# Kernel tuning notes

Measured on AMD Instinct MI355X. Metric: run time of the kernel, lower is better.

Reference implementation:

```python
import jax, jax.numpy as jnp
from jax import lax
import numpy as np

NPOINT = 1024
RADII = (0.1, 0.2, 0.4)
NSAMPLES = (16, 32, 64)
MLPS = ((64, 64, 128), (128, 128, 256), (128, 128, 256))
IN_CH = 64  # 3 (xyz) + 61 (point features)
EPS = 1e-5


def setup_inputs() -> dict:
    key = jax.random.key(0)
    ks = jax.random.split(key, 64)
    inp = {
        "xyz": jax.random.normal(ks[0], (8, 3, 16384), dtype=jnp.float32),
        "points": jax.random.normal(ks[1], (8, 61, 16384), dtype=jnp.float32),
    }
    ki = 2
    for i, mlp in enumerate(MLPS):
        last = IN_CH
        for j, out_ch in enumerate(mlp):
            inp[f"w{i}{j}"] = jax.random.normal(ks[ki], (out_ch, last), dtype=jnp.float32) * 0.05
            inp[f"b{i}{j}"] = jnp.zeros((out_ch,), dtype=jnp.float32)
            inp[f"g{i}{j}"] = jnp.ones((out_ch,), dtype=jnp.float32)
            inp[f"bt{i}{j}"] = jnp.zeros((out_ch,), dtype=jnp.float32)
            last = out_ch
            ki += 1
    return inp


def square_distance(src, dst):
    # src [B,S,3], dst [B,N,3] -> [B,S,N]
    d = -2.0 * jnp.einsum("bsc,bnc->bsn", src, dst)
    d = d + jnp.sum(src * src, -1)[:, :, None]
    d = d + jnp.sum(dst * dst, -1)[:, None, :]
    return d


def farthest_point_sample(xyz, npoint):
    # xyz [B,N,3] -> idx [B,npoint]; deterministic start at index 0
    B, N, _ = xyz.shape
    def step(carry, _):
        distance, farthest = carry
        centroid = jnp.take_along_axis(xyz, farthest[:, None, None], axis=1)  # [B,1,3]
        dist = jnp.sum((xyz - centroid) ** 2, axis=-1)  # [B,N]
        distance = jnp.minimum(distance, dist)
        return (distance, jnp.argmax(distance, axis=-1).astype(jnp.int32)), farthest
    init = (jnp.full((B, N), 1e10, dtype=xyz.dtype), jnp.zeros((B,), dtype=jnp.int32))
    _, idxs = lax.scan(step, init, None, length=npoint)
    return idxs.T  # [B,npoint]


def gather_points(p, idx):
    # p [B,N,C], idx [B,...] -> [B,...,C]
    B = p.shape[0]
    flat = idx.reshape(B, -1)
    g = jnp.take_along_axis(p, flat[:, :, None], axis=1)
    return g.reshape(idx.shape + (p.shape[-1],))


def query_ball_points(radius, nsample, xyz, new_xyz):
    # xyz [B,N,3], new_xyz [B,S,3] -> idx [B,S,nsample]
    B, N, _ = xyz.shape
    d = square_distance(new_xyz, xyz)  # [B,S,N]
    idx = jnp.broadcast_to(jnp.arange(N, dtype=jnp.int32), d.shape)
    idx = jnp.where(d > radius * radius, N, idx)
    idx = jnp.sort(idx, axis=-1)[:, :, :nsample]
    first = idx[:, :, :1]
    return jnp.where(idx == N, first, idx)


def _forward(xyz, points, params):
    xyz_t = jnp.transpose(xyz, (0, 2, 1))       # [B,N,3]
    pts_t = jnp.transpose(points, (0, 2, 1))    # [B,N,D]
    B, N, _ = xyz_t.shape
    fps_idx = farthest_point_sample(xyz_t, NPOINT)
    new_xyz = gather_points(xyz_t, fps_idx)     # [B,S,3]
    feats = []
    for i, (radius, K) in enumerate(zip(RADII, NSAMPLES)):
        gidx = query_ball_points(radius, K, xyz_t, new_xyz)      # [B,S,K]
        grouped_xyz = gather_points(xyz_t, gidx) - new_xyz[:, :, None, :]
        grouped_pts = gather_points(pts_t, gidx)
        x = jnp.concatenate([grouped_xyz, grouped_pts], axis=-1)  # [B,S,K,IN_CH]
        for (w, b, g, bt) in params[i]:
            x = jnp.einsum("bskc,oc->bsko", x, w) + b  # 1x1 conv
            mean = jnp.mean(x, axis=(0, 1, 2))
            var = jnp.var(x, axis=(0, 1, 2))
            x = jax.nn.relu(g * (x - mean) * lax.rsqrt(var + EPS) + bt)
        feats.append(jnp.max(x, axis=2))  # [B,S,Cout]
    new_points = jnp.transpose(jnp.concatenate(feats, axis=-1), (0, 2, 1))  # [B,640,S]
    return jnp.transpose(new_xyz, (0, 2, 1)), new_points


def reference(xyz, points,
              w00, b00, g00, bt00, w01, b01, g01, bt01, w02, b02, g02, bt02,
              w10, b10, g10, bt10, w11, b11, g11, bt11, w12, b12, g12, bt12,
              w20, b20, g20, bt20, w21, b21, g21, bt21, w22, b22, g22, bt22):
    params = [
        [(w00, b00, g00, bt00), (w01, b01, g01, bt01), (w02, b02, g02, bt02)],
        [(w10, b10, g10, bt10), (w11, b11, g11, bt11), (w12, b12, g12, bt12)],
        [(w20, b20, g20, bt20), (w21, b21, g21, bt21), (w22, b22, g22, bt22)],
    ]
    return _forward(xyz, points, params)
```

## Files before the change

kernel.cpp:

```cpp
#include <hip/hip_runtime.h>
#include <stdint.h>

#define BB 8
#define NN 16384
#define SS 1024

typedef unsigned short u16;
typedef float f32x4 __attribute__((ext_vector_type(4)));
typedef short short8v __attribute__((ext_vector_type(8)));
typedef unsigned short us4 __attribute__((ext_vector_type(4)));
typedef unsigned short us8 __attribute__((ext_vector_type(8)));

static __device__ __forceinline__ float bf2f(u16 u){
    union { uint32_t u; float f; } v; v.u = ((uint32_t)u) << 16; return v.f;
}
static __device__ __forceinline__ u16 f2bf(float f){
    union { float f; uint32_t u; } v; v.f = f;
    return (u16)((v.u + 0x7FFFu + ((v.u >> 16) & 1u)) >> 16);
}
static constexpr int cmax2(int a, int b){ return a > b ? a : b; }

#define LP 12288

__global__ __launch_bounds__(1024) void fps_kernel(const float* __restrict__ xyz,
                                                   int* __restrict__ fps_idx){
#pragma clang fp contract(off)
    __shared__ float lx[LP], ly[LP], lz[LP];
    __shared__ unsigned long long slot;
    int b = blockIdx.x;
    int t = threadIdx.x;
    const float* xb = xyz + (size_t)b*3*NN;
    float px[16], py[16], pz[16], dd[16];
#pragma unroll
    for (int j=0;j<16;++j){
        int n = t + j*1024;
        px[j] = xb[n];
        py[j] = xb[NN+n];
        pz[j] = xb[2*NN+n];
        dd[j] = 1e10f;
    }
#pragma unroll
    for (int j=0;j<16;++j){
        asm volatile("" : "+v"(px[j]), "+v"(py[j]), "+v"(pz[j]));
    }
    for (int idx = t; idx < LP; idx += 1024){
        lx[idx] = xb[idx];
        ly[idx] = xb[NN+idx];
        lz[idx] = xb[2*NN+idx];
    }
    if (t == 0) slot = 0ull;
    __syncthreads();

    int lane = t & 63;
    int far = 0;
    int* outp = fps_idx + b*SS;
    float cx = xb[0], cy = xb[NN], cz = xb[2*NN];
    for (int it=0; it<SS; ++it){
        if (t==0) outp[it] = far;
#pragma unroll
        for (int j=0;j<16;++j){
            float dx = px[j]-cx, dy = py[j]-cy, dz = pz[j]-cz;
            float d = dx*dx + dy*dy;
            d = d + dz*dz;
            dd[j] = fminf(dd[j], d);
        }
        float m01 = fmaxf(dd[0], dd[1]),  m23 = fmaxf(dd[2], dd[3]);
        float m45 = fmaxf(dd[4], dd[5]),  m67 = fmaxf(dd[6], dd[7]);
        float m89 = fmaxf(dd[8], dd[9]),  mab = fmaxf(dd[10], dd[11]);
        float mcd = fmaxf(dd[12], dd[13]), mef = fmaxf(dd[14], dd[15]);
        float ma = fmaxf(fmaxf(m01, m23), fmaxf(m45, m67));
        float mb = fmaxf(fmaxf(m89, mab), fmaxf(mcd, mef));
        float mx = fmaxf(ma, mb);
        int bj = 0;
#pragma unroll
        for (int j=15; j>=0; --j){
            if (dd[j] == mx) bj = j;
        }
        int bn = t + (bj << 10);
        unsigned long long pk = ((unsigned long long)(unsigned)(it+1) << 46)
                              | ((unsigned long long)__float_as_uint(mx) << 14)
                              | (unsigned long long)(unsigned)(16383 - bn);
#pragma unroll
        for (int off=32; off>0; off>>=1){
            unsigned long long o = __shfl_down(pk, off);
            pk = (o > pk) ? o : pk;
        }
        if (lane == 0) atomicMax(&slot, pk);
        __syncthreads();
        unsigned long long win = slot;
        far = 16383 - (int)(win & 0x3FFFull);
        if (far < LP){
            cx = lx[far]; cy = ly[far]; cz = lz[far];
        } else {
            cx = xb[far]; cy = xb[NN+far]; cz = xb[2*NN+far];
        }
    }
}

__global__ void gather_q_kernel(const float* __restrict__ xyz, const int* __restrict__ fps_idx,
                                float* __restrict__ q, float* __restrict__ out_xyz){
    int i = blockIdx.x*blockDim.x + threadIdx.x;
    if (i >= BB*SS) return;
    int b = i >> 10, s = i & 1023;
    int idx = fps_idx[i];
    for (int c=0;c<3;++c){
        float v = xyz[((size_t)b*3+c)*NN + idx];
        q[i*3+c] = v;
        out_xyz[((size_t)b*3+c)*SS + s] = v;
    }
}

__global__ __launch_bounds__(256) void build_ptsT_kernel(const float* __restrict__ xyz, const float* __restrict__ pts,
                                                         float* __restrict__ ptsT){
    __shared__ float tile[64][65];
    int b = blockIdx.y;
    int n0 = blockIdx.x * 64;
    int t = threadIdx.x;
    int ln = t & 63, cr = t >> 6;
    for (int c = cr; c < 64; c += 4){
        float v;
        if (c < 3) v = xyz[((size_t)b*3 + c)*NN + n0 + ln];
        else       v = pts[((size_t)b*61 + (c-3))*NN + n0 + ln];
        tile[ln][c] = v;
    }
    __syncthreads();
    int lc = t & 63, nr = t >> 6;
    for (int n = nr; n < 64; n += 4){
        ptsT[((size_t)b*NN + n0 + n)*64 + lc] = tile[n][lc];
    }
}

__global__ __launch_bounds__(256) void ballquery_kernel(const float* __restrict__ xyz, const float* __restrict__ q,
        int* __restrict__ idx0, int* __restrict__ idx1, int* __restrict__ idx2,
        float r2a, float r2b, float r2c){
#pragma clang fp contract(off)
    __shared__ int lds[4][112];
    int t = threadIdx.x;
    int w = t >> 6, lane = t & 63;
    int qi = blockIdx.x*4 + w;
    int b = qi >> 10;
    const float* xb = xyz + (size_t)b*3*NN;
    float qx = q[qi*3], qy = q[qi*3+1], qz = q[qi*3+2];
    float qn = qx*qx + qy*qy; qn = qn + qz*qz;
    int* l0 = lds[w];
    int* l1 = l0 + 16;
    int* l2 = l0 + 48;
    l0[lane] = 0;
    if (lane < 48) l0[64+lane] = 0;
    int c0=0, c1=0, c2=0;
    uint64_t below = (1ull << lane) - 1ull;
    for (int ch=0; ch<256; ++ch){
        int n = ch*64 + lane;
        float x = xb[n], y = xb[NN+n], z = xb[2*NN+n];
        float dn = x*x + y*y; dn = dn + z*z;
        float dot = qx*x + qy*y; dot = dot + qz*z;
        float d = -2.0f*dot + qn;
        d = d + dn;
        bool o0 = d <= r2a, o1 = d <= r2b, o2 = d <= r2c;
        uint64_t m0 = __ballot(o0), m1 = __ballot(o1), m2 = __ballot(o2);
        if (c0 < 16){
            int p = c0 + (int)__popcll(m0 & below);
            if (o0 && p < 16) l0[p] = n;
            c0 += (int)__popcll(m0); if (c0 > 16) c0 = 16;
        }
        if (c1 < 32){
            int p = c1 + (int)__popcll(m1 & below);
            if (o1 && p < 32) l1[p] = n;
            c1 += (int)__popcll(m1); if (c1 > 32) c1 = 32;
        }
        if (c2 < 64){
            int p = c2 + (int)__popcll(m2 & below);
            if (o2 && p < 64) l2[p] = n;
            c2 += (int)__popcll(m2); if (c2 > 64) c2 = 64;
        }
        if (c0>=16 && c1>=32 && c2>=64) break;
    }
    __syncthreads();
    int f0 = l0[0], f1 = l1[0], f2 = l2[0];
    if (lane >= c0 && lane < 16) l0[lane] = f0;
    if (lane >= c1 && lane < 32) l1[lane] = f1;
    if (lane >= c2)              l2[lane] = f2;
    __syncthreads();
    if (lane < 16) idx0[(size_t)qi*16 + lane] = l0[lane];
    if (lane < 32) idx1[(size_t)qi*32 + lane] = l1[lane];
    idx2[(size_t)qi*64 + lane] = l2[lane];
}


template<int CC, int OH>
__device__ __forceinline__ void stage_W(const float* __restrict__ W, char* __restrict__ Wl, int t){
    constexpr int CH = CC/8;
    constexpr int SLOTS = OH*CH;
    for (int s = t; s < SLOTS; s += 256){
        int o = s / CH, kc = s - o*CH;
        const float* wp = W + o*CC + kc*8;
        float4 w0 = *(const float4*)(wp);
        float4 w1 = *(const float4*)(wp+4);
        us8 u;
        u[0]=f2bf(w0.x); u[1]=f2bf(w0.y); u[2]=f2bf(w0.z); u[3]=f2bf(w0.w);
        u[4]=f2bf(w1.x); u[5]=f2bf(w1.y); u[6]=f2bf(w1.z); u[7]=f2bf(w1.w);
        *(us8*)(Wl + o*(CC*2) + ((kc*16) ^ ((o&7)<<4))) = u;
    }
}

template<int K>
__device__ __forceinline__ void stage_A_gather(const float* __restrict__ ptsT, const float* __restrict__ q,
                                               const int* __restrict__ gidx, int m0, int t, char* __restrict__ As){
    int r = t >> 2, q4 = t & 3;
    int m = m0 + r;
    int idx = gidx[m];
    int bs = m / K;
    int b = bs >> 10;
    const float* base = ptsT + ((size_t)b*NN + idx)*64;
    float qx=0.f, qy=0.f, qz=0.f;
    if (q4 == 0){ qx = q[bs*3]; qy = q[bs*3+1]; qz = q[bs*3+2]; }
    int rx = (r & 7) << 4;
#pragma unroll
    for (int ii=0; ii<4; ++ii){
        int c0 = q4*16 + ii*4;
        float4 v = *(const float4*)(base + c0);
        if (q4==0 && ii==0){ v.x -= qx; v.y -= qy; v.z -= qz; }
        us4 u;
        u[0]=f2bf(v.x); u[1]=f2bf(v.y); u[2]=f2bf(v.z); u[3]=f2bf(v.w);
        *(us4*)(As + r*128 + ((c0*2) ^ rx)) = u;
    }
}

template<int OP>
__device__ __forceinline__ void stage_A_z(const u16* __restrict__ zbuf, int m0,
                                          const float* __restrict__ sc, const float* __restrict__ sh,
                                          int t, char* __restrict__ As){
    constexpr int CQ = OP/4;
    for (int s = t; s < 64*CQ; s += 256){
        int r = s / CQ, cq = s - r*CQ;
        us4 zv = *(const us4*)&zbuf[((size_t)(m0+r))*OP + cq*4];
        int c = cq*4;
        us4 u;
        u[0] = f2bf(fmaxf(0.f, bf2f(zv[0])*sc[c+0] + sh[c+0]));
        u[1] = f2bf(fmaxf(0.f, bf2f(zv[1])*sc[c+1] + sh[c+1]));
        u[2] = f2bf(fmaxf(0.f, bf2f(zv[2])*sc[c+2] + sh[c+2]));
        u[3] = f2bf(fmaxf(0.f, bf2f(zv[3])*sc[c+3] + sh[c+3]));
        *(us4*)(As + r*(OP*2) + ((cq*8) ^ ((r&7)<<4))) = u;
    }
}

template<int CC, int OH>
__device__ __forceinline__ void mfma_gemm(const char* __restrict__ As, const char* __restrict__ Wl,
                                          f32x4 (&acc)[4][OH/64], int l, int w){
    constexpr int CCB = CC*2;
    int rl = l & 15, kg = l >> 4;
    const char* ap = As + rl*CCB;
    const char* wp = Wl + (w*(OH/4) + rl)*CCB;
    int axor = (rl & 7) << 4;
#pragma unroll
    for (int ks=0; ks<CC/32; ++ks){
        int karg = ((ks<<6) | (kg<<4)) ^ axor;
        short8v a0 = *(const short8v*)(ap + 0*16*CCB + karg);
        short8v a1 = *(const short8v*)(ap + 1*16*CCB + karg);
        short8v a2 = *(const short8v*)(ap + 2*16*CCB + karg);
        short8v a3 = *(const short8v*)(ap + 3*16*CCB + karg);
#pragma unroll
        for (int tc=0; tc<OH/64; ++tc){
            short8v bf = *(const short8v*)(wp + tc*16*CCB + karg);
            acc[0][tc] = __builtin_amdgcn_mfma_f32_16x16x32_bf16(a0, bf, acc[0][tc], 0,0,0);
            acc[1][tc] = __builtin_amdgcn_mfma_f32_16x16x32_bf16(a1, bf, acc[1][tc], 0,0,0);
            acc[2][tc] = __builtin_amdgcn_mfma_f32_16x16x32_bf16(a2, bf, acc[2][tc], 0,0,0);
            acc[3][tc] = __builtin_amdgcn_mfma_f32_16x16x32_bf16(a3, bf, acc[3][tc], 0,0,0);
        }
    }
}

template<int OH>
__device__ __forceinline__ void bias_mfma(f32x4 (&acc)[4][OH/64], const float* __restrict__ bsrc,
                                          int l, int w, int coff){
#pragma unroll
    for (int tc=0; tc<OH/64; ++tc){
        float bb = bsrc[coff + w*(OH/4) + tc*16 + (l&15)];
#pragma unroll
        for (int tr=0; tr<4; ++tr)
#pragma unroll
        for (int e=0; e<4; ++e) acc[tr][tc][e] += bb;
    }
}

template<int OH, int OT>
__device__ __forceinline__ void zstore_mfma(f32x4 (&acc)[4][OH/64], u16* __restrict__ zbuf,
                                            int m0, int l, int w, int coff){
#pragma unroll
    for (int tr=0; tr<4; ++tr)
#pragma unroll
    for (int e=0; e<4; ++e){
        int row = tr*16 + (l>>4)*4 + e;
#pragma unroll
        for (int tc=0; tc<OH/64; ++tc){
            int c = coff + w*(OH/4) + tc*16 + (l&15);
            zbuf[((size_t)(m0+row))*OT + c] = f2bf(acc[tr][tc][e]);
        }
    }
}

template<int OH, int OT, int K, bool EXT>
__device__ __forceinline__ void stats_mfma(f32x4 (&acc)[4][OH/64], int l, int w, int m0, int blk, int coff,
    float* __restrict__ pS, float* __restrict__ pQ,
    float* __restrict__ gmax, float* __restrict__ gmin){
#pragma unroll
    for (int tc=0; tc<OH/64; ++tc){
        float s1 = 0.f, s2 = 0.f;
        float mxr[4], mnr[4];
#pragma unroll
        for (int tr=0; tr<4; ++tr){
            float v0=acc[tr][tc][0], v1=acc[tr][tc][1], v2=acc[tr][tc][2], v3=acc[tr][tc][3];
            s1 += (v0+v1)+(v2+v3);
            s2 += (v0*v0+v1*v1)+(v2*v2+v3*v3);
            if (EXT){
                mxr[tr] = fmaxf(fmaxf(v0,v1),fmaxf(v2,v3));
                mnr[tr] = fminf(fminf(v0,v1),fminf(v2,v3));
            }
        }
        s1 += __shfl_xor(s1,16); s1 += __shfl_xor(s1,32);
        s2 += __shfl_xor(s2,16); s2 += __shfl_xor(s2,32);
        if (EXT){
#pragma unroll
            for (int tr=0; tr<4; ++tr){
                mxr[tr] = fmaxf(mxr[tr], __shfl_xor(mxr[tr],16));
                mxr[tr] = fmaxf(mxr[tr], __shfl_xor(mxr[tr],32));
                mnr[tr] = fminf(mnr[tr], __shfl_xor(mnr[tr],16));
                mnr[tr] = fminf(mnr[tr], __shfl_xor(mnr[tr],32));
            }
        }
        if (l < 16){
            int c = coff + w*(OH/4) + tc*16 + l;
            pS[(size_t)blk*OT + c] = s1;
            pQ[(size_t)blk*OT + c] = s2;
            if (EXT){
                constexpr int G = 64/K, WG = K/16;
#pragma unroll
                for (int g=0; g<G; ++g){
                    float M1 = mxr[g*WG], M2 = mnr[g*WG];
#pragma unroll
                    for (int ww=1; ww<WG; ++ww){
                        M1 = fmaxf(M1, mxr[g*WG+ww]);
                        M2 = fminf(M2, mnr[g*WG+ww]);
                    }
                    gmax[(size_t)(m0/K + g)*OT + c] = M1;
                    gmin[(size_t)(m0/K + g)*OT + c] = M2;
                }
            }
        }
    }
}

template<int OH>
__device__ __forceinline__ void act_to_As_mfma(f32x4 (&acc)[4][OH/64], const float* __restrict__ bsrc,
    const float* __restrict__ sc, const float* __restrict__ sh, int l, int w, char* __restrict__ As){
#pragma unroll
    for (int tc=0; tc<OH/64; ++tc){
        int c = w*(OH/4) + tc*16 + (l&15);
        float bb = bsrc[c], scv = sc[c], shv = sh[c];
#pragma unroll
        for (int tr=0; tr<4; ++tr)
#pragma unroll
        for (int e=0; e<4; ++e){
            int row = tr*16 + (l>>4)*4 + e;
            float vv = fmaxf(0.f, (acc[tr][tc][e]+bb)*scv + shv);
            *(u16*)(As + row*(OH*2) + ((2*c) ^ ((row&7)<<4))) = f2bf(vv);
        }
    }
}

template<int PHASE, int K, int O1, int O2, int O3>
__global__ __launch_bounds__(256) void fused_mlp(
    const float* __restrict__ ptsT, const float* __restrict__ q, const int* __restrict__ gidx,
    const float* __restrict__ W1, const float* __restrict__ b1,
    const float* __restrict__ W2, const float* __restrict__ b2,
    const float* __restrict__ W3, const float* __restrict__ b3,
    const float* __restrict__ sc1, const float* __restrict__ sh1,
    const float* __restrict__ sc2, const float* __restrict__ sh2,
    float* __restrict__ pS, float* __restrict__ pQ,
    float* __restrict__ gmax, float* __restrict__ gmin,
    u16* __restrict__ zbuf)
{
    constexpr int OH3 = (O3 > 128) ? 128 : O3;
    constexpr int AMX = (PHASE==1) ? 64 : (PHASE==2 ? O1 : (PHASE==3 ? cmax2(O1,O2) : O2));
    constexpr int WMX = (PHASE==1) ? O1*64
                      : (PHASE==2) ? cmax2(O2*O1, O1*64)
                      : (PHASE==3) ? cmax2(cmax2(O1*64, O2*O1), OH3*O2)
                      : OH3*O2;
    __shared__ __align__(16) char smem[64*AMX*2 + WMX*2];
    char* As = smem;
    char* Wl = smem + 64*AMX*2;
    int t = threadIdx.x, l = t & 63, w = t >> 6;
    int m0 = blockIdx.x * 64;

    if constexpr (PHASE == 1){
        stage_A_gather<K>(ptsT, q, gidx, m0, t, As);
        stage_W<64,O1>(W1, Wl, t);
        __syncthreads();
        f32x4 acc[4][O1/64] = {};
        mfma_gemm<64,O1>(As, Wl, acc, l, w);
        bias_mfma<O1>(acc, b1, l, w, 0);
        if (zbuf) zstore_mfma<O1,O1>(acc, zbuf, m0, l, w, 0);
        stats_mfma<O1,O1,K,false>(acc, l, w, m0, blockIdx.x, 0, pS,pQ,gmax,gmin);
        return;
    }

    if constexpr (PHASE == 2){
        if (zbuf){
            stage_A_z<O1>(zbuf, m0, sc1, sh1, t, As);
            stage_W<O1,O2>(W2, Wl, t);
            __syncthreads();
        } else {
            stage_A_gather<K>(ptsT, q, gidx, m0, t, As);
            stage_W<64,O1>(W1, Wl, t);
            __syncthreads();
            f32x4 acc1[4][O1/64] = {};
            mfma_gemm<64,O1>(As, Wl, acc1, l, w);
            __syncthreads();
            act_to_As_mfma<O1>(acc1, b1, sc1, sh1, l, w, As);
            stage_W<O1,O2>(W2, Wl, t);
            __syncthreads();
        }
        f32x4 acc[4][O2/64] = {};
        mfma_gemm<O1,O2>(As, Wl, acc, l, w);
        bias_mfma<O2>(acc, b2, l, w, 0);
        if (zbuf) zstore_mfma<O2,O2>(acc, zbuf, m0, l, w, 0);
        stats_mfma<O2,O2,K,false>(acc, l, w, m0, blockIdx.x, 0, pS,pQ,gmax,gmin);
        return;
    }

    if constexpr (PHASE == 3){
        stage_A_gather<K>(ptsT, q, gidx, m0, t, As);
        stage_W<64,O1>(W1, Wl, t);
        __syncthreads();
        f32x4 acc1[4][O1/64] = {};
        mfma_gemm<64,O1>(As, Wl, acc1, l, w);
        __syncthreads();
        act_to_As_mfma<O1>(acc1, b1, sc1, sh1, l, w, As);
        stage_W<O1,O2>(W2, Wl, t);
        __syncthreads();
        f32x4 acc2[4][O2/64] = {};
        mfma_gemm<O1,O2>(As, Wl, acc2, l, w);
        __syncthreads();
        act_to_As_mfma<O2>(acc2, b2, sc2, sh2, l, w, As);
    } else {
        stage_A_z<O2>(zbuf, m0, sc2, sh2, t, As);
    }

    constexpr int HH = O3/OH3;
#pragma unroll
    for (int h=0; h<HH; ++h){
        stage_W<O2,OH3>(W3 + (size_t)h*OH3*O2, Wl, t);
        __syncthreads();
        f32x4 acc[4][OH3/64] = {};
        mfma_gemm<O2,OH3>(As, Wl, acc, l, w);
        bias_mfma<OH3>(acc, b3, l, w, h*OH3);
        stats_mfma<OH3,O3,K,true>(acc, l, w, m0, blockIdx.x, h*OH3, pS,pQ,gmax,gmin);
        if (h+1 < HH) __syncthreads();
    }
}

__global__ __launch_bounds__(256) void finalize_d_kernel(const float* __restrict__ pS, const float* __restrict__ pQ,
                                      const float* __restrict__ g, const float* __restrict__ bt,
                                      float* __restrict__ sc, float* __restrict__ sh, int nb, double invM){
    __shared__ double red[512];
    int c = blockIdx.x;
    int O = gridDim.x;
    int t = threadIdx.x;
    double S=0.0, Q=0.0;
    for (int v=t; v<nb; v+=256){ S += (double)pS[(size_t)v*O + c]; Q += (double)pQ[(size_t)v*O + c]; }
    red[t]=S; red[256+t]=Q;
    __syncthreads();
    for (int s=128; s>0; s>>=1){
        if (t<s){ red[t]+=red[t+s]; red[256+t]+=red[256+t+s]; }
        __syncthreads();
    }
    if (t==0){
        double mean = red[0]*invM;
        double var  = red[256]*invM - mean*mean;
        double scale = (double)g[c] / sqrt(var + 1e-5);
        sc[c] = (float)scale;
        sh[c] = (float)((double)bt[c] - mean*scale);
    }
}

__global__ void final_out_kernel(const float* __restrict__ gmax, const float* __restrict__ gmin,
                                 const float* __restrict__ sc, const float* __restrict__ sh,
                                 float* __restrict__ outp, int O, int logO, int chbase){
    int gid = blockIdx.x*256 + threadIdx.x;
    int c  = gid & (O-1);
    int bs = gid >> logO;
    int b = bs >> 10, s = bs & 1023;
    float scale = sc[c];
    float v = (scale >= 0.f) ? gmax[gid] : gmin[gid];
    float r = fmaxf(0.f, scale*v + sh[c]);
    outp[((size_t)(b*640 + chbase + c))*SS + s] = r;
}

__global__ void ws_marker_kernel(float* outp, float wsval){ if (threadIdx.x==0) outp[0] = wsval; }

template<int K, int O1, int O2, int O3>
static void run_branch(const float* ptsT, const float* q, const int* gidx,
                       float* pS, float* pQ, float* gmax, float* gmin,
                       float* sc1, float* sh1, float* sc2, float* sh2, float* sc3, float* sh3,
                       u16* z2buf, bool use_z,
                       void* const* d_in, int wbase, float* np_out, int chbase, hipStream_t stream)
{
    const int M = BB*SS*K;
    const int nb = M/64;
    auto wp = [&](int jl, int which)->const float* { return (const float*)d_in[2 + (wbase+jl)*4 + which]; };
    const double invM = 1.0 / (double)M;
    u16* zb = use_z ? z2buf : (u16*)nullptr;

    fused_mlp<1,K,O1,O2,O3><<<nb,256,0,stream>>>(ptsT,q,gidx,
        wp(0,0),wp(0,1), wp(1,0),wp(1,1), wp(2,0),wp(2,1),
        sc1,sh1, sc2,sh2, pS,pQ, gmax,gmin, zb);
    finalize_d_kernel<<<O1,256,0,stream>>>(pS,pQ, wp(0,2), wp(0,3), sc1, sh1, nb, invM);

    fused_mlp<2,K,O1,O2,O3><<<nb,256,0,stream>>>(ptsT,q,gidx,
        wp(0,0),wp(0,1), wp(1,0),wp(1,1), wp(2,0),wp(2,1),
        sc1,sh1, sc2,sh2, pS,pQ, gmax,gmin, zb);
    finalize_d_kernel<<<O2,256,0,stream>>>(pS,pQ, wp(1,2), wp(1,3), sc2, sh2, nb, invM);

    if (use_z){
        fused_mlp<4,K,O1,O2,O3><<<nb,256,0,stream>>>(ptsT,q,gidx,
            wp(0,0),wp(0,1), wp(1,0),wp(1,1), wp(2,0),wp(2,1),
            sc1,sh1, sc2,sh2, pS,pQ, gmax,gmin, z2buf);
    } else {
        fused_mlp<3,K,O1,O2,O3><<<nb,256,0,stream>>>(ptsT,q,gidx,
            wp(0,0),wp(0,1), wp(1,0),wp(1,1), wp(2,0),wp(2,1),
            sc1,sh1, sc2,sh2, pS,pQ, gmax,gmin, nullptr);
    }
    finalize_d_kernel<<<O3,256,0,stream>>>(pS,pQ, wp(2,2), wp(2,3), sc3, sh3, nb, invM);

    final_out_kernel<<<(BB*SS*O3)/256,256,0,stream>>>(gmax,gmin, sc3,sh3, np_out, O3, (O3==256?8:7), chbase);
}

extern "C" void kernel_launch(void* const* d_in, const int* in_sizes, int n_in,
                              void* d_out, int out_size, void* d_ws, size_t ws_size,
                              hipStream_t stream)
{
    const float* xyz = (const float*)d_in[0];
    const float* pts = (const float*)d_in[1];
    float* outp = (float*)d_out;

    char* wsb = (char*)d_ws;
    size_t off = 0;
    auto alloc = [&](size_t bytes) -> void* {
        off = (off + 255) & ~(size_t)255;
        void* p = wsb + off;
        off += bytes;
        return p;
    };
    int*   fps_idx = (int*)  alloc((size_t)BB*SS*4);
    float* q       = (float*)alloc((size_t)BB*SS*3*4);
    int*   idx0    = (int*)  alloc((size_t)BB*SS*16*4);
    int*   idx1    = (int*)  alloc((size_t)BB*SS*32*4);
    int*   idx2    = (int*)  alloc((size_t)BB*SS*64*4);
    float* ptsT    = (float*)alloc((size_t)BB*NN*64*4);
    float* pS      = (float*)alloc((size_t)8192*256*4);
    float* pQ      = (float*)alloc((size_t)8192*256*4);
    float* gmax    = (float*)alloc((size_t)8192*256*4);
    float* gmin    = (float*)alloc((size_t)8192*256*4);
    float* sc1     = (float*)alloc(256*4);
    float* sh1     = (float*)alloc(256*4);
    float* sc2     = (float*)alloc(256*4);
    float* sh2     = (float*)alloc(256*4);
    float* sc3     = (float*)alloc(256*4);
    float* sh3     = (float*)alloc(256*4);

    if (off > ws_size){
        ws_marker_kernel<<<1,64,0,stream>>>(outp, (float)ws_size);
        return;
    }

    u16* z2buf = (u16*)alloc((size_t)BB*SS*64*128*2);
    bool use_z = (off <= ws_size);

    build_ptsT_kernel<<<dim3(NN/64, BB), 256, 0, stream>>>(xyz, pts, ptsT);
    fps_kernel<<<BB, 1024, 0, stream>>>(xyz, fps_idx);
    gather_q_kernel<<<32, 256, 0, stream>>>(xyz, fps_idx, q, outp);

    const float r2a = (float)(0.1*0.1);
    const float r2b = (float)(0.2*0.2);
    const float r2c = (float)(0.4*0.4);
    ballquery_kernel<<<2048, 256, 0, stream>>>(xyz, q, idx0, idx1, idx2, r2a, r2b, r2c);

    float* np_out = outp + (size_t)BB*3*SS;
    run_branch<16, 64, 64,128>(ptsT, q, idx0, pS,pQ, gmax,gmin, sc1,sh1,sc2,sh2,sc3,sh3, z2buf, use_z, d_in, 0, np_out,   0, stream);
    run_branch<32,128,128,256>(ptsT, q, idx1, pS,pQ, gmax,gmin, sc1,sh1,sc2,sh2,sc3,sh3, z2buf, use_z, d_in, 3, np_out, 128, stream);
    run_branch<64,128,128,256>(ptsT, q, idx2, pS,pQ, gmax,gmin, sc1,sh1,sc2,sh2,sc3,sh3, z2buf, use_z, d_in, 6, np_out, 384, stream);

    hipError_t e = hipGetLastError();
    if (e != hipSuccess){
        ws_marker_kernel<<<1,64,0,stream>>>(outp, 1000.0f + (float)(int)e);
    }
}
```

Baseline: 2.798 ms.

## Preconvert MLP weights to bf16 once and load MFMA B fragments into registers

Adds a small kernel that converts all MLP weights to bf16 once per call; the fused MLP kernels then load their weight fragments straight from global memory into registers instead of staging them through LDS. This drops the per-block fp32-to-bf16 conversion and LDS weight traffic, shrinks shared memory use and removes some barriers. The trade-off is much higher register pressure from holding the fragments. Separately, the FPS kernel is rewritten to use 2-wide float vectors (aimed at packed FP32 math) and gains an occupancy hint in its launch bounds.

```diff
diff --git a/kernel.cpp b/kernel.cpp
--- a/kernel.cpp
+++ b/kernel.cpp
@@ -7,6 +7,7 @@
 
 typedef unsigned short u16;
 typedef float f32x4 __attribute__((ext_vector_type(4)));
+typedef float f32x2 __attribute__((ext_vector_type(2)));
 typedef short short8v __attribute__((ext_vector_type(8)));
 typedef unsigned short us4 __attribute__((ext_vector_type(4)));
 typedef unsigned short us8 __attribute__((ext_vector_type(8)));
@@ -22,25 +23,25 @@
 
 #define LP 12288
 
-__global__ __launch_bounds__(1024) void fps_kernel(const float* __restrict__ xyz,
-                                                   int* __restrict__ fps_idx){
+__global__ __launch_bounds__(1024, 4) void fps_kernel(const float* __restrict__ xyz,
+                                                      int* __restrict__ fps_idx){
 #pragma clang fp contract(off)
     __shared__ float lx[LP], ly[LP], lz[LP];
     __shared__ unsigned long long slot;
     int b = blockIdx.x;
     int t = threadIdx.x;
     const float* xb = xyz + (size_t)b*3*NN;
-    float px[16], py[16], pz[16], dd[16];
-#pragma unroll
-    for (int j=0;j<16;++j){
-        int n = t + j*1024;
-        px[j] = xb[n];
-        py[j] = xb[NN+n];
-        pz[j] = xb[2*NN+n];
-        dd[j] = 1e10f;
-    }
-#pragma unroll
-    for (int j=0;j<16;++j){
+    f32x2 px[8], py[8], pz[8], dd[8];
+#pragma unroll
+    for (int j=0;j<8;++j){
+        int n = t + (2*j)*1024;
+        px[j][0] = xb[n];        px[j][1] = xb[n+1024];
+        py[j][0] = xb[NN+n];     py[j][1] = xb[NN+n+1024];
+        pz[j][0] = xb[2*NN+n];   pz[j][1] = xb[2*NN+n+1024];
+        dd[j][0] = 1e10f;        dd[j][1] = 1e10f;
+    }
+#pragma unroll
+    for (int j=0;j<8;++j){
         asm volatile("" : "+v"(px[j]), "+v"(py[j]), "+v"(pz[j]));
     }
     for (int idx = t; idx < LP; idx += 1024){
@@ -57,24 +58,27 @@
     float cx = xb[0], cy = xb[NN], cz = xb[2*NN];
     for (int it=0; it<SS; ++it){
         if (t==0) outp[it] = far;
-#pragma unroll
-        for (int j=0;j<16;++j){
-            float dx = px[j]-cx, dy = py[j]-cy, dz = pz[j]-cz;
-            float d = dx*dx + dy*dy;
+        f32x2 c2x; c2x[0]=cx; c2x[1]=cx;
+        f32x2 c2y; c2y[0]=cy; c2y[1]=cy;
+        f32x2 c2z; c2z[0]=cz; c2z[1]=cz;
+#pragma unroll
+        for (int j=0;j<8;++j){
+            f32x2 dx = px[j]-c2x, dy = py[j]-c2y, dz = pz[j]-c2z;
+            f32x2 d = dx*dx + dy*dy;
             d = d + dz*dz;
-            dd[j] = fminf(dd[j], d);
-        }
-        float m01 = fmaxf(dd[0], dd[1]),  m23 = fmaxf(dd[2], dd[3]);
-        float m45 = fmaxf(dd[4], dd[5]),  m67 = fmaxf(dd[6], dd[7]);
-        float m89 = fmaxf(dd[8], dd[9]),  mab = fmaxf(dd[10], dd[11]);
-        float mcd = fmaxf(dd[12], dd[13]), mef = fmaxf(dd[14], dd[15]);
-        float ma = fmaxf(fmaxf(m01, m23), fmaxf(m45, m67));
-        float mb = fmaxf(fmaxf(m89, mab), fmaxf(mcd, mef));
-        float mx = fmaxf(ma, mb);
+            dd[j][0] = fminf(dd[j][0], d[0]);
+            dd[j][1] = fminf(dd[j][1], d[1]);
+        }
+        float m0 = fmaxf(fmaxf(dd[0][0], dd[0][1]), fmaxf(dd[1][0], dd[1][1]));
+        float m1 = fmaxf(fmaxf(dd[2][0], dd[2][1]), fmaxf(dd[3][0], dd[3][1]));
+        float m2 = fmaxf(fmaxf(dd[4][0], dd[4][1]), fmaxf(dd[5][0], dd[5][1]));
+        float m3 = fmaxf(fmaxf(dd[6][0], dd[6][1]), fmaxf(dd[7][0], dd[7][1]));
+        float mx = fmaxf(fmaxf(m0, m1), fmaxf(m2, m3));
         int bj = 0;
 #pragma unroll
-        for (int j=15; j>=0; --j){
-            if (dd[j] == mx) bj = j;
+        for (int idx=15; idx>=0; --idx){
+            float v = (idx&1) ? dd[idx>>1][1] : dd[idx>>1][0];
+            if (v == mx) bj = idx;
         }
         int bn = t + (bj << 10);
         unsigned long long pk = ((unsigned long long)(unsigned)(it+1) << 46)
@@ -186,20 +190,28 @@
     idx2[(size_t)qi*64 + lane] = l2[lane];
 }
 
+__global__ void convert_w3_kernel(const float* __restrict__ A, int na,
+                                  const float* __restrict__ B, int nbb,
+                                  const float* __restrict__ C, int nc,
+                                  u16* __restrict__ out){
+    int i = blockIdx.x*256 + threadIdx.x;
+    if (i < na) out[i] = f2bf(A[i]);
+    else if (i < na+nbb) out[i] = f2bf(B[i-na]);
+    else if (i < na+nbb+nc) out[i] = f2bf(C[i-na-nbb]);
+}
+
 
 template<int CC, int OH>
-__device__ __forceinline__ void stage_W(const float* __restrict__ W, char* __restrict__ Wl, int t){
-    constexpr int CH = CC/8;
-    constexpr int SLOTS = OH*CH;
-    for (int s = t; s < SLOTS; s += 256){
-        int o = s / CH, kc = s - o*CH;
-        const float* wp = W + o*CC + kc*8;
-        float4 w0 = *(const float4*)(wp);
-        float4 w1 = *(const float4*)(wp+4);
-        us8 u;
-        u[0]=f2bf(w0.x); u[1]=f2bf(w0.y); u[2]=f2bf(w0.z); u[3]=f2bf(w0.w);
-        u[4]=f2bf(w1.x); u[5]=f2bf(w1.y); u[6]=f2bf(w1.z); u[7]=f2bf(w1.w);
-        *(us8*)(Wl + o*(CC*2) + ((kc*16) ^ ((o&7)<<4))) = u;
+__device__ __forceinline__ void load_W_frags(const u16* __restrict__ Wb,
+                                             short8v (&wf)[CC/32][OH/64],
+                                             int l, int w, int hoff){
+    int rl = l & 15, kg = l >> 4;
+#pragma unroll
+    for (int ks=0; ks<CC/32; ++ks)
+#pragma unroll
+    for (int tc=0; tc<OH/64; ++tc){
+        int col = hoff + w*(OH/4) + tc*16 + rl;
+        wf[ks][tc] = *(const short8v*)(Wb + (size_t)col*CC + ks*32 + kg*8);
     }
 }
 
@@ -245,12 +257,12 @@
 }
 
 template<int CC, int OH>
-__device__ __forceinline__ void mfma_gemm(const char* __restrict__ As, const char* __restrict__ Wl,
-                                          f32x4 (&acc)[4][OH/64], int l, int w){
+__device__ __forceinline__ void mfma_gemm_v2(const char* __restrict__ As,
+                                             const short8v (&wf)[CC/32][OH/64],
+                                             f32x4 (&acc)[4][OH/64], int l){
     constexpr int CCB = CC*2;
     int rl = l & 15, kg = l >> 4;
     const char* ap = As + rl*CCB;
-    const char* wp = Wl + (w*(OH/4) + rl)*CCB;
     int axor = (rl & 7) << 4;
 #pragma unroll
     for (int ks=0; ks<CC/32; ++ks){
@@ -261,11 +273,10 @@
         short8v a3 = *(const short8v*)(ap + 3*16*CCB + karg);
 #pragma unroll
         for (int tc=0; tc<OH/64; ++tc){
-            short8v bf = *(const short8v*)(wp + tc*16*CCB + karg);
-            acc[0][tc] = __builtin_amdgcn_mfma_f32_16x16x32_bf16(a0, bf, acc[0][tc], 0,0,0);
-            acc[1][tc] = __builtin_amdgcn_mfma_f32_16x16x32_bf16(a1, bf, acc[1][tc], 0,0,0);
-            acc[2][tc] = __builtin_amdgcn_mfma_f32_16x16x32_bf16(a2, bf, acc[2][tc], 0,0,0);
-            acc[3][tc] = __builtin_amdgcn_mfma_f32_16x16x32_bf16(a3, bf, acc[3][tc], 0,0,0);
+            acc[0][tc] = __builtin_amdgcn_mfma_f32_16x16x32_bf16(a0, wf[ks][tc], acc[0][tc], 0,0,0);
+            acc[1][tc] = __builtin_amdgcn_mfma_f32_16x16x32_bf16(a1, wf[ks][tc], acc[1][tc], 0,0,0);
+            acc[2][tc] = __builtin_amdgcn_mfma_f32_16x16x32_bf16(a2, wf[ks][tc], acc[2][tc], 0,0,0);
+            acc[3][tc] = __builtin_amdgcn_mfma_f32_16x16x32_bf16(a3, wf[ks][tc], acc[3][tc], 0,0,0);
         }
     }
 }
@@ -371,9 +382,9 @@
 template<int PHASE, int K, int O1, int O2, int O3>
 __global__ __launch_bounds__(256) void fused_mlp(
     const float* __restrict__ ptsT, const float* __restrict__ q, const int* __restrict__ gidx,
-    const float* __restrict__ W1, const float* __restrict__ b1,
-    const float* __restrict__ W2, const float* __restrict__ b2,
-    const float* __restrict__ W3, const float* __restrict__ b3,
+    const u16* __restrict__ Wb1, const float* __restrict__ b1,
+    const u16* __restrict__ Wb2, const float* __restrict__ b2,
+    const u16* __restrict__ Wb3, const float* __restrict__ b3,
     const float* __restrict__ sc1, const float* __restrict__ sh1,
     const float* __restrict__ sc2, const float* __restrict__ sh2,
     float* __restrict__ pS, float* __restrict__ pQ,
@@ -382,22 +393,17 @@
 {
     constexpr int OH3 = (O3 > 128) ? 128 : O3;
     constexpr int AMX = (PHASE==1) ? 64 : (PHASE==2 ? O1 : (PHASE==3 ? cmax2(O1,O2) : O2));
-    constexpr int WMX = (PHASE==1) ? O1*64
-                      : (PHASE==2) ? cmax2(O2*O1, O1*64)
-                      : (PHASE==3) ? cmax2(cmax2(O1*64, O2*O1), OH3*O2)
-                      : OH3*O2;
-    __shared__ __align__(16) char smem[64*AMX*2 + WMX*2];
-    char* As = smem;
-    char* Wl = smem + 64*AMX*2;
+    __shared__ __align__(16) char As[64*AMX*2];
     int t = threadIdx.x, l = t & 63, w = t >> 6;
     int m0 = blockIdx.x * 64;
 
     if constexpr (PHASE == 1){
         stage_A_gather<K>(ptsT, q, gidx, m0, t, As);
-        stage_W<64,O1>(W1, Wl, t);
+        short8v wf[2][O1/64];
+        load_W_frags<64,O1>(Wb1, wf, l, w, 0);
         __syncthreads();
         f32x4 acc[4][O1/64] = {};
-        mfma_gemm<64,O1>(As, Wl, acc, l, w);
+        mfma_gemm_v2<64,O1>(As, wf, acc, l);
         bias_mfma<O1>(acc, b1, l, w, 0);
         if (zbuf) zstore_mfma<O1,O1>(acc, zbuf, m0, l, w, 0);
         stats_mfma<O1,O1,K,false>(acc, l, w, m0, blockIdx.x, 0, pS,pQ,gmax,gmin);
@@ -407,21 +413,21 @@
     if constexpr (PHASE == 2){
         if (zbuf){
             stage_A_z<O1>(zbuf, m0, sc1, sh1, t, As);
-            stage_W<O1,O2>(W2, Wl, t);
-            __syncthreads();
         } else {
             stage_A_gather<K>(ptsT, q, gidx, m0, t, As);
-            stage_W<64,O1>(W1, Wl, t);
+            short8v wf1[2][O1/64];
+            load_W_frags<64,O1>(Wb1, wf1, l, w, 0);
             __syncthreads();
             f32x4 acc1[4][O1/64] = {};
-            mfma_gemm<64,O1>(As, Wl, acc1, l, w);
+            mfma_gemm_v2<64,O1>(As, wf1, acc1, l);
             __syncthreads();
             act_to_As_mfma<O1>(acc1, b1, sc1, sh1, l, w, As);
-            stage_W<O1,O2>(W2, Wl, t);
-            __syncthreads();
-        }
+        }
+        short8v wf[O1/32][O2/64];
+        load_W_frags<O1,O2>(Wb2, wf, l, w, 0);
+        __syncthreads();
         f32x4 acc[4][O2/64] = {};
-        mfma_gemm<O1,O2>(As, Wl, acc, l, w);
+        mfma_gemm_v2<O1,O2>(As, wf, acc, l);
         bias_mfma<O2>(acc, b2, l, w, 0);
         if (zbuf) zstore_mfma<O2,O2>(acc, zbuf, m0, l, w, 0);
         stats_mfma<O2,O2,K,false>(acc, l, w, m0, blockIdx.x, 0, pS,pQ,gmax,gmin);
@@ -430,32 +436,34 @@
 
     if constexpr (PHASE == 3){
         stage_A_gather<K>(ptsT, q, gidx, m0, t, As);
-        stage_W<64,O1>(W1, Wl, t);
+        short8v wf1[2][O1/64];
+        load_W_frags<64,O1>(Wb1, wf1, l, w, 0);
         __syncthreads();
         f32x4 acc1[4][O1/64] = {};
-        mfma_gemm<64,O1>(As, Wl, acc1, l, w);
+        mfma_gemm_v2<64,O1>(As, wf1, acc1, l);
         __syncthreads();
         act_to_As_mfma<O1>(acc1, b1, sc1, sh1, l, w, As);
-        stage_W<O1,O2>(W2, Wl, t);
-        __syncthreads();
+        __syncthreads();
+        short8v wf2[O1/32][O2/64];
+        load_W_frags<O1,O2>(Wb2, wf2, l, w, 0);
         f32x4 acc2[4][O2/64] = {};
-        mfma_gemm<O1,O2>(As, Wl, acc2, l, w);
+        mfma_gemm_v2<O1,O2>(As, wf2, acc2, l);
         __syncthreads();
         act_to_As_mfma<O2>(acc2, b2, sc2, sh2, l, w, As);
     } else {
         stage_A_z<O2>(zbuf, m0, sc2, sh2, t, As);
     }
 
+    __syncthreads();
     constexpr int HH = O3/OH3;
 #pragma unroll
     for (int h=0; h<HH; ++h){
-        stage_W<O2,OH3>(W3 + (size_t)h*OH3*O2, Wl, t);
-        __syncthreads();
+        short8v wf[O2/32][OH3/64];
+        load_W_frags<O2,OH3>(Wb3, wf, l, w, h*OH3);
         f32x4 acc[4][OH3/64] = {};
-        mfma_gemm<O2,OH3>(As, Wl, acc, l, w);
+        mfma_gemm_v2<O2,OH3>(As, wf, acc, l);
         bias_mfma<OH3>(acc, b3, l, w, h*OH3);
         stats_mfma<OH3,O3,K,true>(acc, l, w, m0, blockIdx.x, h*OH3, pS,pQ,gmax,gmin);
-        if (h+1 < HH) __syncthreads();
     }
 }
 
@@ -502,7 +510,7 @@
 static void run_branch(const float* ptsT, const float* q, const int* gidx,
                        float* pS, float* pQ, float* gmax, float* gmin,
                        float* sc1, float* sh1, float* sc2, float* sh2, float* sc3, float* sh3,
-                       u16* z2buf, bool use_z,
+                       u16* z2buf, bool use_z, const u16* wb,
                        void* const* d_in, int wbase, float* np_out, int chbase, hipStream_t stream)
 {
     const int M = BB*SS*K;
@@ -510,24 +518,27 @@
     auto wp = [&](int jl, int which)->const float* { return (const float*)d_in[2 + (wbase+jl)*4 + which]; };
     const double invM = 1.0 / (double)M;
     u16* zb = use_z ? z2buf : (u16*)nullptr;
+    const u16* Wb1 = wb;
+    const u16* Wb2 = wb + (size_t)O1*64;
+    const u16* Wb3 = wb + (size_t)O1*64 + (size_t)O2*O1;
 
     fused_mlp<1,K,O1,O2,O3><<<nb,256,0,stream>>>(ptsT,q,gidx,
-        wp(0,0),wp(0,1), wp(1,0),wp(1,1), wp(2,0),wp(2,1),
+        Wb1,wp(0,1), Wb2,wp(1,1), Wb3,wp(2,1),
         sc1,sh1, sc2,sh2, pS,pQ, gmax,gmin, zb);
     finalize_d_kernel<<<O1,256,0,stream>>>(pS,pQ, wp(0,2), wp(0,3), sc1, sh1, nb, invM);
 
     fused_mlp<2,K,O1,O2,O3><<<nb,256,0,stream>>>(ptsT,q,gidx,
-        wp(0,0),wp(0,1), wp(1,0),wp(1,1), wp(2,0),wp(2,1),
+        Wb1,wp(0,1), Wb2,wp(1,1), Wb3,wp(2,1),
         sc1,sh1, sc2,sh2, pS,pQ, gmax,gmin, zb);
     finalize_d_kernel<<<O2,256,0,stream>>>(pS,pQ, wp(1,2), wp(1,3), sc2, sh2, nb, invM);
 
     if (use_z){
         fused_mlp<4,K,O1,O2,O3><<<nb,256,0,stream>>>(ptsT,q,gidx,
-            wp(0,0),wp(0,1), wp(1,0),wp(1,1), wp(2,0),wp(2,1),
+            Wb1,wp(0,1), Wb2,wp(1,1), Wb3,wp(2,1),
             sc1,sh1, sc2,sh2, pS,pQ, gmax,gmin, z2buf);
     } else {
         fused_mlp<3,K,O1,O2,O3><<<nb,256,0,stream>>>(ptsT,q,gidx,
-            wp(0,0),wp(0,1), wp(1,0),wp(1,1), wp(2,0),wp(2,1),
+            Wb1,wp(0,1), Wb2,wp(1,1), Wb3,wp(2,1),
             sc1,sh1, sc2,sh2, pS,pQ, gmax,gmin, nullptr);
     }
     finalize_d_kernel<<<O3,256,0,stream>>>(pS,pQ, wp(2,2), wp(2,3), sc3, sh3, nb, invM);
@@ -567,6 +578,9 @@
     float* sh2     = (float*)alloc(256*4);
     float* sc3     = (float*)alloc(256*4);
     float* sh3     = (float*)alloc(256*4);
+    u16*   wbf0    = (u16*)  alloc((size_t)16384*2);
+    u16*   wbf1    = (u16*)  alloc((size_t)57344*2);
+    u16*   wbf2    = (u16*)  alloc((size_t)57344*2);
 
     if (off > ws_size){
         ws_marker_kernel<<<1,64,0,stream>>>(outp, (float)ws_size);
@@ -575,6 +589,11 @@
 
     u16* z2buf = (u16*)alloc((size_t)BB*SS*64*128*2);
     bool use_z = (off <= ws_size);
+
+    auto wptr = [&](int layer)->const float* { return (const float*)d_in[2 + layer*4 + 0]; };
+    convert_w3_kernel<<<64, 256, 0, stream>>>(wptr(0), 4096, wptr(1), 4096, wptr(2), 8192, wbf0);
+    convert_w3_kernel<<<224, 256, 0, stream>>>(wptr(3), 8192, wptr(4), 16384, wptr(5), 32768, wbf1);
+    convert_w3_kernel<<<224, 256, 0, stream>>>(wptr(6), 8192, wptr(7), 16384, wptr(8), 32768, wbf2);
 
     build_ptsT_kernel<<<dim3(NN/64, BB), 256, 0, stream>>>(xyz, pts, ptsT);
     fps_kernel<<<BB, 1024, 0, stream>>>(xyz, fps_idx);
@@ -586,9 +605,9 @@
     ballquery_kernel<<<2048, 256, 0, stream>>>(xyz, q, idx0, idx1, idx2, r2a, r2b, r2c);
 
     float* np_out = outp + (size_t)BB*3*SS;
-    run_branch<16, 64, 64,128>(ptsT, q, idx0, pS,pQ, gmax,gmin, sc1,sh1,sc2,sh2,sc3,sh3, z2buf, use_z, d_in, 0, np_out,   0, stream);
-    run_branch<32,128,128,256>(ptsT, q, idx1, pS,pQ, gmax,gmin, sc1,sh1,sc2,sh2,sc3,sh3, z2buf, use_z, d_in, 3, np_out, 128, stream);
-    run_branch<64,128,128,256>(ptsT, q, idx2, pS,pQ, gmax,gmin, sc1,sh1,sc2,sh2,sc3,sh3, z2buf, use_z, d_in, 6, np_out, 384, stream);
+    run_branch<16, 64, 64,128>(ptsT, q, idx0, pS,pQ, gmax,gmin, sc1,sh1,sc2,sh2,sc3,sh3, z2buf, use_z, wbf0, d_in, 0, np_out,   0, stream);
+    run_branch<32,128,128,256>(ptsT, q, idx1, pS,pQ, gmax,gmin, sc1,sh1,sc2,sh2,sc3,sh3, z2buf, use_z, wbf1, d_in, 3, np_out, 128, stream);
+    run_branch<64,128,128,256>(ptsT, q, idx2, pS,pQ, gmax,gmin, sc1,sh1,sc2,sh2,sc3,sh3, z2buf, use_z, wbf2, d_in, 6, np_out, 384, stream);
 
     hipError_t e = hipGetLastError();
     if (e != hipSuccess){
```

New measurement: 2.734 ms. -2.3%, faster.
